# Kernel optimization log

Measured on AMD Instinct MI355X. Metric: run time of the kernel, lower is better.

## Reference

```python
import jax, jax.numpy as jnp
import numpy as np

H = 56; W = 56; WS = 7; SS = 3; NH = 6; C = 192; B = 32
T = H * W; HD = C // NH; NW = (H // WS) * (W // WS); TW = WS * WS
SCALE = HD ** -0.5


def _rel_index():
    # relative position index per WindowAttentionLayer.calculate_coordinates
    coords = np.stack(np.meshgrid(np.arange(WS), np.arange(WS), indexing='ij')).reshape(2, -1)
    rel = (coords[:, :, None] - coords[:, None, :]).transpose(1, 2, 0).astype(np.int64)
    rel[:, :, 0] += WS - 1
    rel[:, :, 1] += WS - 1
    rel[:, :, 0] *= 2 * WS - 1
    return rel.sum(-1).reshape(-1)  # [TW*TW]


def _attn_mask():
    # shifted-window attention mask, per WindowAttentionBlock.__init__
    img = np.zeros((H, W))
    slices = (slice(0, -WS), slice(-WS, -SS), slice(-SS, None))
    cnt = 0
    for hs in slices:
        for ws_ in slices:
            img[hs, ws_] = cnt
            cnt += 1
    mw = img.reshape(H // WS, WS, W // WS, WS).transpose(0, 2, 1, 3).reshape(-1, TW)
    am = mw[:, None, :] - mw[:, :, None]
    return np.where(am != 0, np.float32(-100.0), np.float32(0.0))  # [NW, TW, TW]


_REL = jnp.asarray(_rel_index())
_MASK = jnp.asarray(_attn_mask())


def _ln(x, g, b):
    m = x.mean(-1, keepdims=True)
    v = ((x - m) ** 2).mean(-1, keepdims=True)
    return (x - m) * jax.lax.rsqrt(v + 1e-5) * g + b


def setup_inputs() -> dict:
    key = jax.random.key(0)
    ks = jax.random.split(key, 8)
    s = 0.02
    return {
        'x': jax.random.normal(ks[0], (B, T, C), jnp.float32),
        'ln1_g': jnp.ones((C,), jnp.float32),
        'ln1_b': jnp.zeros((C,), jnp.float32),
        'qkv_w': jax.random.normal(ks[1], (C, 3 * C), jnp.float32) * s,
        'qkv_b': jnp.zeros((3 * C,), jnp.float32),
        'pos_bias': jax.random.normal(ks[2], ((2 * WS - 1) * (2 * WS - 1), NH), jnp.float32) * s,
        'proj_w': jax.random.normal(ks[3], (C, C), jnp.float32) * s,
        'proj_b': jnp.zeros((C,), jnp.float32),
        'ln2_g': jnp.ones((C,), jnp.float32),
        'ln2_b': jnp.zeros((C,), jnp.float32),
        'mlp_w1': jax.random.normal(ks[4], (C, 4 * C), jnp.float32) * s,
        'mlp_b1': jnp.zeros((4 * C,), jnp.float32),
        'mlp_w2': jax.random.normal(ks[5], (4 * C, C), jnp.float32) * s,
        'mlp_b2': jnp.zeros((C,), jnp.float32),
    }


def reference(x, ln1_g, ln1_b, qkv_w, qkv_b, pos_bias, proj_w, proj_b,
              ln2_g, ln2_b, mlp_w1, mlp_b1, mlp_w2, mlp_b2):
    shortcut = x
    h = _ln(x, ln1_g, ln1_b).reshape(B, H, W, C)
    h = jnp.roll(h, (-SS, -SS), axis=(1, 2))  # cyclic shift
    # window partition -> [B*NW, TW, C]
    h = h.reshape(B, H // WS, WS, W // WS, WS, C).transpose(0, 1, 3, 2, 4, 5).reshape(B * NW, TW, C)
    qkv = (h @ qkv_w + qkv_b).reshape(B * NW, TW, 3, NH, HD).transpose(2, 0, 3, 1, 4)
    q, k, v = qkv[0] * SCALE, qkv[1], qkv[2]  # [B*NW, NH, TW, HD]
    attn = jnp.einsum('nhid,nhjd->nhij', q, k)  # [B*NW, NH, TW, TW]
    bias = pos_bias[_REL].reshape(TW, TW, NH).transpose(2, 0, 1)  # [NH, TW, TW]
    attn = attn + bias[None]
    attn = (attn.reshape(B, NW, NH, TW, TW) + _MASK[None, :, None]).reshape(B * NW, NH, TW, TW)
    # NOTE: the source forward never applies softmax (self.softmax is unused) -- replicated faithfully
    o = jnp.einsum('nhij,nhjd->nhid', attn, v).transpose(0, 2, 1, 3).reshape(B * NW, TW, C)
    o = o @ proj_w + proj_b
    # window reverse + reverse shift
    o = o.reshape(B, H // WS, W // WS, WS, WS, C).transpose(0, 1, 3, 2, 4, 5).reshape(B, H, W, C)
    o = jnp.roll(o, (SS, SS), axis=(1, 2)).reshape(B, T, C)
    x1 = shortcut + o
    m = _ln(x1, ln2_g, ln2_b)
    m = jax.nn.gelu(m @ mlp_w1 + mlp_b1, approximate=False) @ mlp_w2 + mlp_b2
    return x1 + m
```

## Files before the change

kernel.cpp:

```cpp
#include <hip/hip_runtime.h>
#include <hip/hip_bf16.h>

typedef __attribute__((ext_vector_type(8))) short short8;
typedef __attribute__((ext_vector_type(4))) float floatx4;

#define SCALE_Q 0.17677669529663687f

__device__ __forceinline__ short f2bf(float f) {
  union { float f; unsigned u; } a; a.f = f;
  unsigned r = (a.u + 0x7FFFu + ((a.u >> 16) & 1u)) >> 16;
  return (short)r;
}

__device__ __forceinline__ int spatial_row(int r) {
  int n = r / 49, tw = r - n * 49;
  int bb = n >> 6, wdx = n & 63;
  int rh = (wdx >> 3) * 7 + tw / 7, rw = (wdx & 7) * 7 + tw % 7;
  int oh = rh + 3; if (oh >= 56) oh -= 56;
  int ow = rw + 3; if (ow >= 56) ow -= 56;
  return bb * 3136 + oh * 56 + ow;
}

__global__ void transpose_w_k(const float* __restrict__ src, short* __restrict__ dst,
                              int K, int N) {
  int i = blockIdx.x * 256 + threadIdx.x;
  if (i >= N * K) return;
  int n = i / K, k = i - n * K;
  dst[i] = f2bf(src[(size_t)k * N + n]);
}

__global__ void prep_bm_k(const float* __restrict__ pos_bias, float* __restrict__ bm) {
  int i = blockIdx.x * 256 + threadIdx.x;
  if (i >= 64 * 6 * 49 * 49) return;
  int j = i % 49; int t = i / 49; int ii = t % 49; t /= 49; int h = t % 6; int w = t / 6;
  int ih = ii / 7, iw = ii - ih * 7, jh = j / 7, jw = j - jh * 7;
  int rel = (ih - jh + 6) * 13 + (iw - jw + 6);
  float v = pos_bias[rel * 6 + h];
  int wh = w >> 3, ww = w & 7;
  int ri = wh * 7 + ih, ci = ww * 7 + iw, rj = wh * 7 + jh, cj = ww * 7 + jw;
  int regi = ((ri >= 49) + (ri >= 53)) * 3 + ((ci >= 49) + (ci >= 53));
  int regj = ((rj >= 49) + (rj >= 53)) * 3 + ((cj >= 49) + (cj >= 53));
  if (regi != regj) v -= 100.0f;
  bm[i] = v;
}

__global__ __launch_bounds__(256) void ln_k(const float* __restrict__ x,
    const float* __restrict__ g, const float* __restrict__ bta,
    short* __restrict__ outb) {
  int wid = threadIdx.x >> 6, lane = threadIdx.x & 63;
  int r = blockIdx.x * 4 + wid;
  int n = r / 49, tw = r - n * 49;
  int bb = n >> 6, wdx = n & 63;
  int rh = (wdx >> 3) * 7 + tw / 7, rw = (wdx & 7) * 7 + tw % 7;
  int sh = rh + 3; if (sh >= 56) sh -= 56;
  int sw = rw + 3; if (sw >= 56) sw -= 56;
  size_t src = ((size_t)bb * 3136 + sh * 56 + sw) * 192;
  const float* xr = x + src;
  float v0 = xr[lane], v1 = xr[lane + 64], v2 = xr[lane + 128];
  float s = v0 + v1 + v2, sq = v0 * v0 + v1 * v1 + v2 * v2;
  #pragma unroll
  for (int o = 32; o >= 1; o >>= 1) { s += __shfl_xor(s, o); sq += __shfl_xor(sq, o); }
  float mean = s * (1.0f / 192.0f);
  float rstd = rsqrtf(sq * (1.0f / 192.0f) - mean * mean + 1e-5f);
  short* orow = outb + (size_t)r * 192;
  orow[lane]       = f2bf((v0 - mean) * rstd * g[lane]       + bta[lane]);
  orow[lane + 64]  = f2bf((v1 - mean) * rstd * g[lane + 64]  + bta[lane + 64]);
  orow[lane + 128] = f2bf((v2 - mean) * rstd * g[lane + 128] + bta[lane + 128]);
}

template<int EPI>
__global__ __launch_bounds__(256) void pgemm_k(
    const short* __restrict__ A, const short* __restrict__ Bt,
    const float* __restrict__ bias, void* __restrict__ outp,
    const void* __restrict__ aux, int N, int K) {
  __shared__ short As[128][72];
  __shared__ short Bs[64][72];
  int tid = threadIdx.x;
  int gmb = blockIdx.y * 128;
  int gnb = blockIdx.x * 64;
  int wid = tid >> 6, lane = tid & 63;
  int wm = wid >> 1, wn = wid & 1;
  int lr = lane & 15, lk = (lane >> 4) << 3, lq = (lane >> 4) << 2;
  int ar = tid >> 3, ac = (tid & 7) << 3;

  floatx4 acc[4][2];
  #pragma unroll
  for (int i = 0; i < 4; ++i)
    #pragma unroll
    for (int j = 0; j < 2; ++j) acc[i][j] = (floatx4)(0.0f);

  short8 pa[4], pb[2];
  #pragma unroll
  for (int i = 0; i < 4; ++i)
    pa[i] = *(const short8*)&A[(size_t)(gmb + ar + 32 * i) * K + ac];
  #pragma unroll
  for (int i = 0; i < 2; ++i)
    pb[i] = *(const short8*)&Bt[(size_t)(gnb + ar + 32 * i) * K + ac];

  for (int k0 = 0; k0 < K; k0 += 64) {
    #pragma unroll
    for (int i = 0; i < 4; ++i) *(short8*)&As[ar + 32 * i][ac] = pa[i];
    #pragma unroll
    for (int i = 0; i < 2; ++i) *(short8*)&Bs[ar + 32 * i][ac] = pb[i];
    __syncthreads();
    if (k0 + 64 < K) {
      #pragma unroll
      for (int i = 0; i < 4; ++i)
        pa[i] = *(const short8*)&A[(size_t)(gmb + ar + 32 * i) * K + k0 + 64 + ac];
      #pragma unroll
      for (int i = 0; i < 2; ++i)
        pb[i] = *(const short8*)&Bt[(size_t)(gnb + ar + 32 * i) * K + k0 + 64 + ac];
    }
    #pragma unroll
    for (int kk = 0; kk < 64; kk += 32) {
      short8 af[4], bfr[2];
      #pragma unroll
      for (int mi = 0; mi < 4; ++mi)
        af[mi] = *(const short8*)&As[wm * 64 + mi * 16 + lr][kk + lk];
      #pragma unroll
      for (int ni = 0; ni < 2; ++ni)
        bfr[ni] = *(const short8*)&Bs[wn * 32 + ni * 16 + lr][kk + lk];
      #pragma unroll
      for (int mi = 0; mi < 4; ++mi)
        #pragma unroll
        for (int ni = 0; ni < 2; ++ni)
          acc[mi][ni] = __builtin_amdgcn_mfma_f32_16x16x32_bf16(af[mi], bfr[ni], acc[mi][ni], 0, 0, 0);
    }
    __syncthreads();
  }

  #pragma unroll
  for (int mi = 0; mi < 4; ++mi)
    #pragma unroll
    for (int ni = 0; ni < 2; ++ni)
      #pragma unroll
      for (int r = 0; r < 4; ++r) {
        int grow = gmb + wm * 64 + mi * 16 + lq + r;
        int gcol = gnb + wn * 32 + ni * 16 + lr;
        float v = acc[mi][ni][r] + bias[gcol];
        if (EPI == 0) {
          int which = gcol / 192, rem = gcol - which * 192;
          if (which == 0) v *= SCALE_Q;
          int head = rem >> 5, d = rem & 31;
          int n = grow / 49, tw = grow - n * 49;
          ((short*)outp)[((((size_t)(n * 6 + head) * 3 + which) * 49 + tw) << 5) + d] = f2bf(v);
        } else if (EPI == 2) {
          float ge = 0.5f * v * (1.0f + erff(v * 0.70710678118f));
          ((short*)outp)[(size_t)grow * 768 + gcol] = f2bf(ge);
        } else {
          size_t idx = (size_t)grow * 192 + gcol;
          ((float*)outp)[idx] = ((const float*)aux)[idx] + v;
        }
      }
}

__global__ __launch_bounds__(256) void attn_k(const short* __restrict__ qkv,
    const float* __restrict__ bm, short* __restrict__ obuf) {
  __shared__ short lds[4][6912];
  int wid = threadIdx.x >> 6, lane = threadIdx.x & 63;
  int pair = blockIdx.x * 4 + wid;
  int n = pair / 6, h = pair - n * 6;
  short* Vt = &lds[wid][0];
  short* Ps = &lds[wid][32 * 72];
  const short* Qb = qkv + (size_t)((n * 6 + h) * 3) * 1568;
  const short* Kb = Qb + 1568;
  const short* Vb = Qb + 3136;
  int lr = lane & 15, lk = (lane >> 4) << 3, lq = (lane >> 4) << 2;

  #pragma unroll
  for (int it = 0; it < 8; ++it) {
    int u = lane + 64 * it;
    Vt[(u >> 4) * 72 + 48 + (u & 15)] = 0;
  }
  #pragma unroll
  for (int it = 0; it < 4; ++it) {
    int u = lane + 64 * it;
    if (u < 196) {
      int tw = u >> 2, db = (u & 3) << 3;
      short8 vv = *(const short8*)&Vb[tw * 32 + db];
      #pragma unroll
      for (int j = 0; j < 8; ++j) Vt[(db + j) * 72 + tw] = vv[j];
    }
  }

  short8 qf[4], kf[4];
  #pragma unroll
  for (int mi = 0; mi < 4; ++mi)
    qf[mi] = *(const short8*)&Qb[(mi * 16 + lr) * 32 + lk];
  #pragma unroll
  for (int nj = 0; nj < 4; ++nj)
    kf[nj] = *(const short8*)&Kb[(nj * 16 + lr) * 32 + lk];
  floatx4 s[4][4];
  #pragma unroll
  for (int mi = 0; mi < 4; ++mi)
    #pragma unroll
    for (int nj = 0; nj < 4; ++nj)
      s[mi][nj] = __builtin_amdgcn_mfma_f32_16x16x32_bf16(qf[mi], kf[nj], (floatx4)(0.0f), 0, 0, 0);

  const float* bmw = bm + (size_t)((n & 63) * 6 + h) * 2401;
  #pragma unroll
  for (int mi = 0; mi < 4; ++mi)
    #pragma unroll
    for (int nj = 0; nj < 4; ++nj)
      #pragma unroll
      for (int r = 0; r < 4; ++r) {
        int i = mi * 16 + lq + r;
        int j = nj * 16 + lr;
        float v = 0.0f;
        if (i < 49 && j < 49) v = s[mi][nj][r] + bmw[i * 49 + j];
        Ps[i * 72 + j] = f2bf(v);
      }

  floatx4 o[4][2];
  #pragma unroll
  for (int mi = 0; mi < 4; ++mi)
    #pragma unroll
    for (int ni = 0; ni < 2; ++ni) o[mi][ni] = (floatx4)(0.0f);
  #pragma unroll
  for (int kc = 0; kc < 2; ++kc) {
    short8 pf[4], vf[2];
    #pragma unroll
    for (int mi = 0; mi < 4; ++mi)
      pf[mi] = *(const short8*)&Ps[(mi * 16 + lr) * 72 + kc * 32 + lk];
    #pragma unroll
    for (int ni = 0; ni < 2; ++ni)
      vf[ni] = *(const short8*)&Vt[(ni * 16 + lr) * 72 + kc * 32 + lk];
    #pragma unroll
    for (int mi = 0; mi < 4; ++mi)
      #pragma unroll
      for (int ni = 0; ni < 2; ++ni)
        o[mi][ni] = __builtin_amdgcn_mfma_f32_16x16x32_bf16(pf[mi], vf[ni], o[mi][ni], 0, 0, 0);
  }
  #pragma unroll
  for (int mi = 0; mi < 4; ++mi)
    #pragma unroll
    for (int ni = 0; ni < 2; ++ni)
      #pragma unroll
      for (int r = 0; r < 4; ++r) {
        int i = mi * 16 + lq + r;
        if (i < 49)
          obuf[((size_t)n * 49 + i) * 192 + h * 32 + ni * 16 + lr] = f2bf(o[mi][ni][r]);
      }
}

__global__ __launch_bounds__(512) void proj_ln2_k(
    const short* __restrict__ obuf, const short* __restrict__ projT,
    const float* __restrict__ proj_b, const float* __restrict__ x,
    const float* __restrict__ g2, const float* __restrict__ bt2,
    float* __restrict__ x1out, short* __restrict__ ln2out) {
  __shared__ short As[128][72];
  __shared__ short Bs[192][72];
  __shared__ float sums[128][4][2];
  __shared__ float stats[128][2];
  int tid = threadIdx.x;
  int wid = tid >> 6, lane = tid & 63;
  int wm = wid >> 2, wn = wid & 3;
  int lr = lane & 15, lk = (lane >> 4) << 3, lq = (lane >> 4) << 2;
  int R0 = blockIdx.x * 128;
  int ar = tid >> 3, ac = (tid & 7) << 3;

  floatx4 acc[4][3];
  #pragma unroll
  for (int mi = 0; mi < 4; ++mi)
    #pragma unroll
    for (int ni = 0; ni < 3; ++ni) acc[mi][ni] = (floatx4)(0.0f);

  short8 pa[2], pbr[3];
  #pragma unroll
  for (int i = 0; i < 2; ++i)
    pa[i] = *(const short8*)&obuf[(size_t)(R0 + ar + 64 * i) * 192 + ac];
  #pragma unroll
  for (int i = 0; i < 3; ++i)
    pbr[i] = *(const short8*)&projT[(size_t)(ar + 64 * i) * 192 + ac];

  for (int k0 = 0; k0 < 192; k0 += 64) {
    #pragma unroll
    for (int i = 0; i < 2; ++i) *(short8*)&As[ar + 64 * i][ac] = pa[i];
    #pragma unroll
    for (int i = 0; i < 3; ++i) *(short8*)&Bs[ar + 64 * i][ac] = pbr[i];
    __syncthreads();
    if (k0 < 128) {
      #pragma unroll
      for (int i = 0; i < 2; ++i)
        pa[i] = *(const short8*)&obuf[(size_t)(R0 + ar + 64 * i) * 192 + k0 + 64 + ac];
      #pragma unroll
      for (int i = 0; i < 3; ++i)
        pbr[i] = *(const short8*)&projT[(size_t)(ar + 64 * i) * 192 + k0 + 64 + ac];
    }
    #pragma unroll
    for (int kk = 0; kk < 64; kk += 32) {
      short8 af[4], bfr[3];
      #pragma unroll
      for (int mi = 0; mi < 4; ++mi)
        af[mi] = *(const short8*)&As[wm * 64 + mi * 16 + lr][kk + lk];
      #pragma unroll
      for (int ni = 0; ni < 3; ++ni)
        bfr[ni] = *(const short8*)&Bs[wn * 48 + ni * 16 + lr][kk + lk];
      #pragma unroll
      for (int mi = 0; mi < 4; ++mi)
        #pragma unroll
        for (int ni = 0; ni < 3; ++ni)
          acc[mi][ni] = __builtin_amdgcn_mfma_f32_16x16x32_bf16(af[mi], bfr[ni], acc[mi][ni], 0, 0, 0);
    }
    __syncthreads();
  }

  int col[3]; float pb[3], gv[3], bv[3];
  #pragma unroll
  for (int ni = 0; ni < 3; ++ni) {
    col[ni] = wn * 48 + ni * 16 + lr;
    pb[ni] = proj_b[col[ni]];
    gv[ni] = g2[col[ni]];
    bv[ni] = bt2[col[ni]];
  }

  int srw[4][4];
  #pragma unroll
  for (int mi = 0; mi < 4; ++mi)
    #pragma unroll
    for (int rr = 0; rr < 4; ++rr) {
      int row_l = wm * 64 + mi * 16 + lq + rr;
      int sr = spatial_row(R0 + row_l);
      srw[mi][rr] = sr;
      float s = 0.0f, sq = 0.0f;
      #pragma unroll
      for (int ni = 0; ni < 3; ++ni) {
        float v = acc[mi][ni][rr] + pb[ni] + x[(size_t)sr * 192 + col[ni]];
        acc[mi][ni][rr] = v;
        s += v; sq += v * v;
      }
      #pragma unroll
      for (int o = 8; o >= 1; o >>= 1) { s += __shfl_xor(s, o); sq += __shfl_xor(sq, o); }
      if (lr == 0) { sums[row_l][wn][0] = s; sums[row_l][wn][1] = sq; }
    }
  __syncthreads();
  if (tid < 128) {
    float s = sums[tid][0][0] + sums[tid][1][0] + sums[tid][2][0] + sums[tid][3][0];
    float sq = sums[tid][0][1] + sums[tid][1][1] + sums[tid][2][1] + sums[tid][3][1];
    float mean = s * (1.0f / 192.0f);
    float var = sq * (1.0f / 192.0f) - mean * mean;
    stats[tid][0] = mean;
    stats[tid][1] = rsqrtf(var + 1e-5f);
  }
  __syncthreads();

  #pragma unroll
  for (int mi = 0; mi < 4; ++mi)
    #pragma unroll
    for (int rr = 0; rr < 4; ++rr) {
      int row_l = wm * 64 + mi * 16 + lq + rr;
      int sr = srw[mi][rr];
      float mean = stats[row_l][0], rstd = stats[row_l][1];
      #pragma unroll
      for (int ni = 0; ni < 3; ++ni) {
        float v = acc[mi][ni][rr];
        x1out[(size_t)sr * 192 + col[ni]] = v;
        ln2out[(size_t)sr * 192 + col[ni]] = f2bf((v - mean) * rstd * gv[ni] + bv[ni]);
      }
    }
}

extern "C" void kernel_launch(void* const* d_in, const int* in_sizes, int n_in,
                              void* d_out, int out_size, void* d_ws, size_t ws_size,
                              hipStream_t stream) {
  const float* x      = (const float*)d_in[0];
  const float* ln1_g  = (const float*)d_in[1];
  const float* ln1_b  = (const float*)d_in[2];
  const float* qkv_w  = (const float*)d_in[3];
  const float* qkv_b  = (const float*)d_in[4];
  const float* pos_b  = (const float*)d_in[5];
  const float* proj_w = (const float*)d_in[6];
  const float* proj_b = (const float*)d_in[7];
  const float* ln2_g  = (const float*)d_in[8];
  const float* ln2_b  = (const float*)d_in[9];
  const float* mlp_w1 = (const float*)d_in[10];
  const float* mlp_b1 = (const float*)d_in[11];
  const float* mlp_w2 = (const float*)d_in[12];
  const float* mlp_b2 = (const float*)d_in[13];

  char* ws = (char*)d_ws;
  short* qkvbuf  = (short*)(ws);
  short* hidden  = (short*)(ws);
  short* obuf    = (short*)(ws + 115605504);
  short* hbuf    = (short*)(ws + 154140672);
  short* ln2b    = (short*)(ws + 154140672);
  short* wT      = (short*)(ws + 192675840);
  short* qkv_wT  = wT;
  short* proj_wT = wT + 110592;
  short* m1_wT   = wT + 110592 + 36864;
  short* m2_wT   = wT + 110592 + 36864 + 147456;
  float* bm      = (float*)(ws + 193560576);
  float* xout    = (float*)d_out;

  transpose_w_k<<<(110592 + 255) / 256, 256, 0, stream>>>(qkv_w,  qkv_wT, 192, 576);
  transpose_w_k<<<(36864  + 255) / 256, 256, 0, stream>>>(proj_w, proj_wT, 192, 192);
  transpose_w_k<<<(147456 + 255) / 256, 256, 0, stream>>>(mlp_w1, m1_wT,  192, 768);
  transpose_w_k<<<(147456 + 255) / 256, 256, 0, stream>>>(mlp_w2, m2_wT,  768, 192);
  prep_bm_k<<<(64 * 6 * 2401 + 255) / 256, 256, 0, stream>>>(pos_b, bm);

  ln_k<<<25088, 256, 0, stream>>>(x, ln1_g, ln1_b, hbuf);
  pgemm_k<0><<<dim3(9, 784),  256, 0, stream>>>(hbuf, qkv_wT, qkv_b, qkvbuf, nullptr, 576, 192);
  attn_k<<<3072, 256, 0, stream>>>(qkvbuf, bm, obuf);
  proj_ln2_k<<<784, 512, 0, stream>>>(obuf, proj_wT, proj_b, x, ln2_g, ln2_b, xout, ln2b);
  pgemm_k<2><<<dim3(12, 784), 256, 0, stream>>>(ln2b, m1_wT, mlp_b1, hidden, nullptr, 768, 192);
  pgemm_k<3><<<dim3(3, 784),  256, 0, stream>>>(hidden, m2_wT, mlp_b2, xout, xout, 192, 768);
}
```

Baseline: 498.6 us.

## Fuse LN1 into QKV GEMM and remap GEMM grids with XCD-aware swizzle

LayerNorm1 and the QKV projection now run in one kernel: each block normalizes 64 shifted-window rows straight into LDS and multiplies them against a 64-column weight tile. This removes the bf16 intermediate buffer write and read, plus one launch. The cost is that each row's LN is recomputed by the 9 column blocks. The MLP GEMMs move to a 1D grid with a block-index swizzle that gives each of the 8 XCDs a contiguous range of tiles, aiming for better L2 reuse.

```diff
diff --git a/kernel.cpp b/kernel.cpp
--- a/kernel.cpp
+++ b/kernel.cpp
@@ -44,40 +44,100 @@
   bm[i] = v;
 }
 
-__global__ __launch_bounds__(256) void ln_k(const float* __restrict__ x,
-    const float* __restrict__ g, const float* __restrict__ bta,
-    short* __restrict__ outb) {
-  int wid = threadIdx.x >> 6, lane = threadIdx.x & 63;
-  int r = blockIdx.x * 4 + wid;
-  int n = r / 49, tw = r - n * 49;
-  int bb = n >> 6, wdx = n & 63;
-  int rh = (wdx >> 3) * 7 + tw / 7, rw = (wdx & 7) * 7 + tw % 7;
-  int sh = rh + 3; if (sh >= 56) sh -= 56;
-  int sw = rw + 3; if (sw >= 56) sw -= 56;
-  size_t src = ((size_t)bb * 3136 + sh * 56 + sw) * 192;
-  const float* xr = x + src;
-  float v0 = xr[lane], v1 = xr[lane + 64], v2 = xr[lane + 128];
-  float s = v0 + v1 + v2, sq = v0 * v0 + v1 * v1 + v2 * v2;
-  #pragma unroll
-  for (int o = 32; o >= 1; o >>= 1) { s += __shfl_xor(s, o); sq += __shfl_xor(sq, o); }
-  float mean = s * (1.0f / 192.0f);
-  float rstd = rsqrtf(sq * (1.0f / 192.0f) - mean * mean + 1e-5f);
-  short* orow = outb + (size_t)r * 192;
-  orow[lane]       = f2bf((v0 - mean) * rstd * g[lane]       + bta[lane]);
-  orow[lane + 64]  = f2bf((v1 - mean) * rstd * g[lane + 64]  + bta[lane + 64]);
-  orow[lane + 128] = f2bf((v2 - mean) * rstd * g[lane + 128] + bta[lane + 128]);
+__global__ __launch_bounds__(256) void ln1qkv_k(
+    const float* __restrict__ x, const float* __restrict__ g1, const float* __restrict__ bt1,
+    const short* __restrict__ qkv_wT, const float* __restrict__ bias,
+    short* __restrict__ outp) {
+  __shared__ short As[64][200];
+  __shared__ short Bs[64][72];
+  int per8 = gridDim.x >> 3;
+  int sid = (blockIdx.x & 7) * per8 + (blockIdx.x >> 3);
+  int R0  = (sid / 9) * 64;
+  int gnb = (sid % 9) * 64;
+  int tid = threadIdx.x, wid = tid >> 6, lane = tid & 63;
+  int lr = lane & 15, lk = (lane >> 4) << 3, lq = (lane >> 4) << 2;
+
+  for (int rr = wid; rr < 64; rr += 4) {
+    int r = R0 + rr;
+    int n = r / 49, tw = r - n * 49;
+    int bb = n >> 6, wdx = n & 63;
+    int rh = (wdx >> 3) * 7 + tw / 7, rw = (wdx & 7) * 7 + tw % 7;
+    int sh = rh + 3; if (sh >= 56) sh -= 56;
+    int sw = rw + 3; if (sw >= 56) sw -= 56;
+    const float* xr = x + ((size_t)bb * 3136 + sh * 56 + sw) * 192;
+    float v0 = xr[lane], v1 = xr[lane + 64], v2 = xr[lane + 128];
+    float s = v0 + v1 + v2, sq = v0 * v0 + v1 * v1 + v2 * v2;
+    #pragma unroll
+    for (int o = 32; o >= 1; o >>= 1) { s += __shfl_xor(s, o); sq += __shfl_xor(sq, o); }
+    float mean = s * (1.0f / 192.0f);
+    float rstd = rsqrtf(sq * (1.0f / 192.0f) - mean * mean + 1e-5f);
+    As[rr][lane]       = f2bf((v0 - mean) * rstd * g1[lane]       + bt1[lane]);
+    As[rr][lane + 64]  = f2bf((v1 - mean) * rstd * g1[lane + 64]  + bt1[lane + 64]);
+    As[rr][lane + 128] = f2bf((v2 - mean) * rstd * g1[lane + 128] + bt1[lane + 128]);
+  }
+
+  int ar = tid >> 3, ac = (tid & 7) << 3;
+  short8 pb[2];
+  #pragma unroll
+  for (int i = 0; i < 2; ++i)
+    pb[i] = *(const short8*)&qkv_wT[(size_t)(gnb + ar + 32 * i) * 192 + ac];
+  __syncthreads();
+
+  floatx4 acc[4];
+  #pragma unroll
+  for (int i = 0; i < 4; ++i) acc[i] = (floatx4)(0.0f);
+
+  for (int k0 = 0; k0 < 192; k0 += 64) {
+    #pragma unroll
+    for (int i = 0; i < 2; ++i) *(short8*)&Bs[ar + 32 * i][ac] = pb[i];
+    __syncthreads();
+    if (k0 < 128) {
+      #pragma unroll
+      for (int i = 0; i < 2; ++i)
+        pb[i] = *(const short8*)&qkv_wT[(size_t)(gnb + ar + 32 * i) * 192 + k0 + 64 + ac];
+    }
+    #pragma unroll
+    for (int kk = 0; kk < 64; kk += 32) {
+      short8 af[4], bfr;
+      #pragma unroll
+      for (int mi = 0; mi < 4; ++mi)
+        af[mi] = *(const short8*)&As[mi * 16 + lr][k0 + kk + lk];
+      bfr = *(const short8*)&Bs[wid * 16 + lr][kk + lk];
+      #pragma unroll
+      for (int mi = 0; mi < 4; ++mi)
+        acc[mi] = __builtin_amdgcn_mfma_f32_16x16x32_bf16(af[mi], bfr, acc[mi], 0, 0, 0);
+    }
+    __syncthreads();
+  }
+
+  int gcol = gnb + wid * 16 + lr;
+  int which = gcol / 192, rem = gcol - which * 192;
+  int head = rem >> 5, d = rem & 31;
+  float bv = bias[gcol];
+  #pragma unroll
+  for (int mi = 0; mi < 4; ++mi)
+    #pragma unroll
+    for (int r = 0; r < 4; ++r) {
+      int grow = R0 + mi * 16 + lq + r;
+      float v = acc[mi][r] + bv;
+      if (which == 0) v *= SCALE_Q;
+      int n = grow / 49, tw = grow - n * 49;
+      outp[((((size_t)(n * 6 + head) * 3 + which) * 49 + tw) << 5) + d] = f2bf(v);
+    }
 }
 
 template<int EPI>
 __global__ __launch_bounds__(256) void pgemm_k(
     const short* __restrict__ A, const short* __restrict__ Bt,
     const float* __restrict__ bias, void* __restrict__ outp,
-    const void* __restrict__ aux, int N, int K) {
+    const void* __restrict__ aux, int NB, int K) {
   __shared__ short As[128][72];
   __shared__ short Bs[64][72];
+  int per8 = gridDim.x >> 3;
+  int sid = (blockIdx.x & 7) * per8 + (blockIdx.x >> 3);
+  int gmb = (sid / NB) * 128;
+  int gnb = (sid % NB) * 64;
   int tid = threadIdx.x;
-  int gmb = blockIdx.y * 128;
-  int gnb = blockIdx.x * 64;
   int wid = tid >> 6, lane = tid & 63;
   int wm = wid >> 1, wn = wid & 1;
   int lr = lane & 15, lk = (lane >> 4) << 3, lq = (lane >> 4) << 2;
@@ -138,13 +198,7 @@
         int grow = gmb + wm * 64 + mi * 16 + lq + r;
         int gcol = gnb + wn * 32 + ni * 16 + lr;
         float v = acc[mi][ni][r] + bias[gcol];
-        if (EPI == 0) {
-          int which = gcol / 192, rem = gcol - which * 192;
-          if (which == 0) v *= SCALE_Q;
-          int head = rem >> 5, d = rem & 31;
-          int n = grow / 49, tw = grow - n * 49;
-          ((short*)outp)[((((size_t)(n * 6 + head) * 3 + which) * 49 + tw) << 5) + d] = f2bf(v);
-        } else if (EPI == 2) {
+        if (EPI == 2) {
           float ge = 0.5f * v * (1.0f + erff(v * 0.70710678118f));
           ((short*)outp)[(size_t)grow * 768 + gcol] = f2bf(ge);
         } else {
@@ -382,7 +436,6 @@
   short* qkvbuf  = (short*)(ws);
   short* hidden  = (short*)(ws);
   short* obuf    = (short*)(ws + 115605504);
-  short* hbuf    = (short*)(ws + 154140672);
   short* ln2b    = (short*)(ws + 154140672);
   short* wT      = (short*)(ws + 192675840);
   short* qkv_wT  = wT;
@@ -398,10 +451,9 @@
   transpose_w_k<<<(147456 + 255) / 256, 256, 0, stream>>>(mlp_w2, m2_wT,  768, 192);
   prep_bm_k<<<(64 * 6 * 2401 + 255) / 256, 256, 0, stream>>>(pos_b, bm);
 
-  ln_k<<<25088, 256, 0, stream>>>(x, ln1_g, ln1_b, hbuf);
-  pgemm_k<0><<<dim3(9, 784),  256, 0, stream>>>(hbuf, qkv_wT, qkv_b, qkvbuf, nullptr, 576, 192);
+  ln1qkv_k<<<14112, 256, 0, stream>>>(x, ln1_g, ln1_b, qkv_wT, qkv_b, qkvbuf);
   attn_k<<<3072, 256, 0, stream>>>(qkvbuf, bm, obuf);
   proj_ln2_k<<<784, 512, 0, stream>>>(obuf, proj_wT, proj_b, x, ln2_g, ln2_b, xout, ln2b);
-  pgemm_k<2><<<dim3(12, 784), 256, 0, stream>>>(ln2b, m1_wT, mlp_b1, hidden, nullptr, 768, 192);
-  pgemm_k<3><<<dim3(3, 784),  256, 0, stream>>>(hidden, m2_wT, mlp_b2, xout, xout, 192, 768);
-}
+  pgemm_k<2><<<9408, 256, 0, stream>>>(ln2b, m1_wT, mlp_b1, hidden, nullptr, 12, 192);
+  pgemm_k<3><<<2352, 256, 0, stream>>>(hidden, m2_wT, mlp_b2, xout, xout, 3, 768);
+}
```

After: 715.2 us. +43.4%, slower.
